# Performance work log

Hardware: AMD Instinct MI355X
Metric: run time of the kernel (lower is better)

## Reference

```python
import jax, jax.numpy as jnp
import numpy as np

EPS = 1e-5
COMMIT_W = 2.0
LATENT = 64


def _conv1d(x, w, b, stride, padding):
    # x: [B,C,T], w: [O,I,K] (torch Conv1d layout)
    y = jax.lax.conv_general_dilated(x, w, (stride,), [(padding, padding)],
                                     dimension_numbers=('NCH', 'OIH', 'NCH'))
    return y + b[None, :, None]


def _bn(x, g, b):
    # training-mode BatchNorm1d: batch statistics over (B, T) per channel
    mu = x.mean(axis=(0, 2), keepdims=True)
    var = x.var(axis=(0, 2), keepdims=True)
    return (x - mu) * jax.lax.rsqrt(var + EPS) * g[None, :, None] + b[None, :, None]


def setup_inputs():
    key = jax.random.key(0)
    ks = jax.random.split(key, 10)
    B, T, D, K = 8, 10240, LATENT, 8192
    f32 = jnp.float32
    def n(k, shape, scale):
        return jax.random.normal(k, shape, dtype=f32) * scale
    return {
        'x': jax.random.normal(ks[0], (B, 1, T), dtype=f32),
        'enc_w1': n(ks[1], (16, 1, 5), 0.3), 'enc_b1': jnp.zeros((16,), f32),
        'bn1_g': jnp.ones((16,), f32), 'bn1_b': jnp.zeros((16,), f32),
        'enc_w2': n(ks[2], (32, 16, 5), 0.1), 'enc_b2': jnp.zeros((32,), f32),
        'bn2_g': jnp.ones((32,), f32), 'bn2_b': jnp.zeros((32,), f32),
        'enc_w3': n(ks[3], (64, 32, 25), 0.05), 'enc_b3': jnp.zeros((64,), f32),
        'bn3_g': jnp.ones((64,), f32), 'bn3_b': jnp.zeros((64,), f32),
        'codebook': jax.random.normal(ks[4], (K, D), dtype=f32),
        'dec_wt': n(ks[5], (64, 64, 25), 0.05),  # torch ConvTranspose1d [in,out,k]
        'dbn1_g': jnp.ones((64,), f32), 'dbn1_b': jnp.zeros((64,), f32),
        'dec_w2': n(ks[6], (64, 64, 5), 0.08), 'dec_b2': jnp.zeros((64,), f32),
        'dbn2_g': jnp.ones((64,), f32), 'dbn2_b': jnp.zeros((64,), f32),
        'dec_w3': n(ks[7], (1, 64, 1), 0.1), 'dec_b3': jnp.zeros((1,), f32),
    }


def reference(x, enc_w1, enc_b1, bn1_g, bn1_b, enc_w2, enc_b2, bn2_g, bn2_b,
              enc_w3, enc_b3, bn3_g, bn3_b, codebook, dec_wt, dbn1_g, dbn1_b,
              dec_w2, dec_b2, dbn2_g, dbn2_b, dec_w3, dec_b3):
    # ---- encoder ----
    h = jax.nn.silu(_conv1d(x, enc_w1, enc_b1, 1, 2))
    h = _bn(h, bn1_g, bn1_b)
    h = jax.nn.silu(_conv1d(h, enc_w2, enc_b2, 1, 2))
    h = _bn(h, bn2_g, bn2_b)
    h = jnp.tanh(_conv1d(h, enc_w3, enc_b3, 5, 12))
    z = _bn(h, bn3_g, bn3_b)                       # [B, 64, L]
    B, _, L = z.shape
    # ---- VQ: euclidean nearest-neighbor against codebook ----
    zf = z.transpose(0, 2, 1).reshape(-1, LATENT)  # [N, D]
    d = ((zf * zf).sum(-1, keepdims=True)
         - 2.0 * zf @ codebook.T
         + (codebook * codebook).sum(-1)[None, :])  # [N, K]
    idx = jnp.argmin(d, axis=-1)                   # [N]
    q = codebook[idx]                              # [N, D]
    commit_loss = COMMIT_W * jnp.mean((jax.lax.stop_gradient(q) - zf) ** 2)
    q_st = zf + jax.lax.stop_gradient(q - zf)      # straight-through
    zq = q_st.reshape(B, L, LATENT).transpose(0, 2, 1)  # [B, 64, L]
    # ---- decoder ----
    # ConvTranspose1d(k=25, s=5, p=12) == dilated conv with flipped kernel
    wconv = jnp.flip(dec_wt, -1).transpose(1, 0, 2)     # [out, in, k]
    h = jax.lax.conv_general_dilated(zq, wconv, (1,), [(12, 12)], lhs_dilation=(5,),
                                     dimension_numbers=('NCH', 'OIH', 'NCH'))
    h = jax.nn.silu(h)
    h = _bn(h, dbn1_g, dbn1_b)
    h = jax.nn.silu(_conv1d(h, dec_w2, dec_b2, 1, 2))
    h = _bn(h, dbn2_g, dbn2_b)
    recon = _conv1d(h, dec_w3, dec_b3, 1, 0)       # [B, 1, ~T]
    T = x.shape[2]
    cur = recon.shape[2]
    if cur > T:
        recon = recon[:, :, :T]
    elif cur < T:
        recon = jnp.pad(recon, ((0, 0), (0, 0), (0, T - cur)))
    return recon, idx.reshape(B, L), commit_loss
```

## Files before the change

kernel.cpp:

```cpp
#include <hip/hip_runtime.h>
#include <hip/hip_bf16.h>

#define DEV __device__ __forceinline__

typedef __attribute__((ext_vector_type(8))) short s8v;
typedef __attribute__((ext_vector_type(16))) float f32x16;
typedef __attribute__((address_space(1))) const unsigned int u32g;
typedef __attribute__((address_space(3))) unsigned int u32l;

DEV void gl_lds(const void* g, void* l){
  __builtin_amdgcn_global_load_lds((u32g*)g, (u32l*)l, 16, 0, 0);
}

DEV float siluf(float x){ return x / (1.f + expf(-x)); }

DEV float wredsum(float v){
  #pragma unroll
  for(int m = 32; m; m >>= 1) v += __shfl_xor(v, m);
  return v;
}

DEV unsigned short bf16rne(float f){
  unsigned int u = __float_as_uint(f);
  u += 0x7FFFu + ((u >> 16) & 1u);
  return (unsigned short)(u >> 16);
}
DEV float bf16tof(unsigned short h){ return __uint_as_float(((unsigned int)h) << 16); }

DEV unsigned umed3(unsigned a, unsigned b, unsigned c){
  unsigned d;
  asm("v_med3_u32 %0, %1, %2, %3" : "=v"(d) : "v"(a), "v"(b), "v"(c));
  return d;
}

#define S1 0
#define Q1 16
#define S2 32
#define Q2 64
#define S3 96
#define Q3 160
#define S4 224
#define Q4 288
#define S5 352
#define Q5 416
#define SLOSS 480
#define NSTATF 512

#define EPSQ 6u
#define NCHUNK 8

__global__ void k_prep(const float* ew3, const float* dwt, float* w3t, float* dwtt,
                       unsigned short* wb7){
  const int n1 = 64*32*25, n2 = 64*64*25;
  for(int i = blockIdx.x*blockDim.x + threadIdx.x; i < n1+n2; i += gridDim.x*blockDim.x){
    if(i < n1){
      int c = i/(32*25), r = i - c*(32*25), ii = r/25, k = r - ii*25;
      w3t[(ii*25 + k)*64 + c] = ew3[i];
    } else {
      int j = i - n1;
      int ii = j/(64*25), r = j - ii*(64*25), o = r/25, k = r - o*25;
      float w = dwt[j];
      dwtt[(ii*25 + k)*64 + o] = w;
      wb7[((size_t)(k*64 + o))*64 + ii] = bf16rne(w);
    }
  }
}

__global__ void k_prep2(const float* __restrict__ cb, unsigned short* __restrict__ cbsw,
                        float* __restrict__ cnw, float* __restrict__ cnw2,
                        unsigned short* __restrict__ cbb, int* cnt){
  if(blockIdx.x == 0 && threadIdx.x == 0) *cnt = 0;
  int j = blockIdx.x*256 + threadIdx.x;
  if(j < 8192){
    float nrm = 0.f;
    unsigned swz = (j & 15) << 4;
    char* rowp = (char*)cbsw + (size_t)j*256;
    #pragma unroll
    for(int k = 0; k < 64; k++){
      float x = cb[(size_t)j*64 + k];
      unsigned short hi = bf16rne(x);
      float lo = x - bf16tof(hi);
      *(unsigned short*)(rowp + (((unsigned)(2*k)) ^ swz)) = hi;
      *(unsigned short*)(rowp + (((unsigned)(128 + 2*k)) ^ swz)) = bf16rne(lo);
      cbb[(size_t)j*64 + k] = hi;
      nrm = fmaf(x, x, nrm);
    }
    cnw[j] = nrm;
    cnw2[j] = (nrm + 1024.f) * 256.f;
  }
}

__global__ void k1(const float* __restrict__ x, const float* __restrict__ w1,
                   const float* __restrict__ b1, float* __restrict__ h1, float* stats){
  __shared__ float xs[260];
  __shared__ float ssum[16], ssq[16];
  int tid = threadIdx.x, b = blockIdx.y, t0 = blockIdx.x*256;
  if(tid < 16){ ssum[tid] = 0.f; ssq[tid] = 0.f; }
  for(int i = tid; i < 260; i += 256){
    int t = t0 + i - 2;
    xs[i] = (t >= 0 && t < 10240) ? x[b*10240 + t] : 0.f;
  }
  __syncthreads();
  int t = t0 + tid;
  #pragma unroll
  for(int c = 0; c < 16; c++){
    float a = b1[c];
    #pragma unroll
    for(int k = 0; k < 5; k++) a = fmaf(w1[c*5+k], xs[tid+k], a);
    a = siluf(a);
    h1[((b*16 + c)*10240) + t] = a;
    float s = wredsum(a), s2 = wredsum(a*a);
    if((tid & 63) == 0){ atomicAdd(&ssum[c], s); atomicAdd(&ssq[c], s2); }
  }
  __syncthreads();
  if(tid < 16){ atomicAdd(stats+S1+tid, ssum[tid]); atomicAdd(stats+Q1+tid, ssq[tid]); }
}

__global__ void k2(const float* __restrict__ h1, const float* __restrict__ w2,
                   const float* __restrict__ b2, const float* __restrict__ g1,
                   const float* __restrict__ bb1, float* __restrict__ h2out, float* stats){
  __shared__ float hs[16*264];
  __shared__ float wl[2560];
  __shared__ float A1[16], B1[16];
  __shared__ float ssum[32], ssq[32];
  int tid = threadIdx.x, b = blockIdx.y, t0 = blockIdx.x*256;
  for(int i = tid; i < 2560; i += 256) wl[i] = w2[i];
  if(tid < 16){
    float mu = stats[S1+tid]/81920.f;
    float var = stats[Q1+tid]/81920.f - mu*mu;
    float rs = rsqrtf(var + 1e-5f);
    A1[tid] = rs*g1[tid];
    B1[tid] = bb1[tid] - mu*rs*g1[tid];
  }
  if(tid < 32){ ssum[tid] = 0.f; ssq[tid] = 0.f; }
  __syncthreads();
  for(int i = tid; i < 16*260; i += 256){
    int ch = i/260, tt = i - ch*260;
    int t = t0 + tt - 2;
    hs[ch*264 + tt] = (t >= 0 && t < 10240) ? (h1[((b*16+ch)*10240)+t]*A1[ch] + B1[ch]) : 0.f;
  }
  __syncthreads();
  int t = t0 + tid;
  float acc[32];
  #pragma unroll
  for(int c = 0; c < 32; c++) acc[c] = b2[c];
  for(int i = 0; i < 16; i++){
    float z0 = hs[i*264+tid], z1 = hs[i*264+tid+1], z2 = hs[i*264+tid+2],
          z3 = hs[i*264+tid+3], z4 = hs[i*264+tid+4];
    #pragma unroll
    for(int c = 0; c < 32; c++){
      const float* wp = &wl[(c*16+i)*5];
      acc[c] = fmaf(wp[0],z0,fmaf(wp[1],z1,fmaf(wp[2],z2,fmaf(wp[3],z3,fmaf(wp[4],z4,acc[c])))));
    }
  }
  #pragma unroll
  for(int c = 0; c < 32; c++){
    float a = siluf(acc[c]);
    h2out[((b*32 + c)*10240) + t] = a;
    float s = wredsum(a), s2 = wredsum(a*a);
    if((tid & 63) == 0){ atomicAdd(&ssum[c], s); atomicAdd(&ssq[c], s2); }
  }
  __syncthreads();
  if(tid < 32){ atomicAdd(stats+S2+tid, ssum[tid]); atomicAdd(stats+Q2+tid, ssq[tid]); }
}

__global__ void k3(const float* __restrict__ h2, const float* __restrict__ w3t,
                   const float* __restrict__ eb3, const float* __restrict__ g2,
                   const float* __restrict__ bb2, float* __restrict__ zn, float* stats){
  __shared__ __align__(16) float X[5*32*24];
  __shared__ float A2[32], B2[32];
  __shared__ float ssum[64], ssq[64];
  int tid = threadIdx.x, b = blockIdx.y, l0 = blockIdx.x*16;
  if(tid < 32){
    float mu = stats[S2+tid]/81920.f;
    float var = stats[Q2+tid]/81920.f - mu*mu;
    float rs = rsqrtf(var + 1e-5f);
    A2[tid] = rs*g2[tid];
    B2[tid] = bb2[tid] - mu*rs*g2[tid];
  }
  if(tid < 64){ ssum[tid] = 0.f; ssq[tid] = 0.f; }
  __syncthreads();
  for(int i2 = tid; i2 < 5*32*20; i2 += 256){
    int kk = i2/640;
    int r  = i2 - kk*640;
    int ch = r/20, m = r - ch*20;
    int t = 5*(l0 + m) + kk - 12;
    float v = 0.f;
    if(t >= 0 && t < 10240) v = h2[((b*32+ch)*10240)+t]*A2[ch] + B2[ch];
    X[(kk*32+ch)*24 + m] = v;
  }
  __syncthreads();
  int c = tid & 63, lslot = tid >> 6;
  float acc[4];
  float bias = eb3[c];
  #pragma unroll
  for(int s = 0; s < 4; s++) acc[s] = bias;
  for(int i = 0; i < 32; i++){
    #pragma unroll
    for(int kk = 0; kk < 5; kk++){
      const float* xp = &X[(kk*32+i)*24 + lslot*4];
      float4 za = *(const float4*)(xp);
      float4 zb = *(const float4*)(xp + 4);
      float z[8] = {za.x,za.y,za.z,za.w,zb.x,zb.y,zb.z,zb.w};
      #pragma unroll
      for(int kap = 0; kap < 5; kap++){
        float w = w3t[(i*25 + kap*5 + kk)*64 + c];
        #pragma unroll
        for(int s = 0; s < 4; s++) acc[s] = fmaf(w, z[s+kap], acc[s]);
      }
    }
  }
  float ls = 0.f, lq = 0.f;
  #pragma unroll
  for(int s = 0; s < 4; s++){
    int l = l0 + lslot*4 + s;
    float a = tanhf(acc[s]);
    zn[((b*2048 + l)*64) + c] = a;
    ls += a; lq += a*a;
  }
  atomicAdd(&ssum[c], ls); atomicAdd(&ssq[c], lq);
  __syncthreads();
  if(tid < 64){ atomicAdd(stats+S3+tid, ssum[tid]); atomicAdd(stats+Q3+tid, ssq[tid]); }
}

__global__ void k3b(float* zn, const float* g3, const float* b3, const float* stats){
  __shared__ float A[64], B[64];
  int tid = threadIdx.x;
  if(tid < 64){
    float mu = stats[S3+tid]/16384.f;
    float var = stats[Q3+tid]/16384.f - mu*mu;
    float rs = rsqrtf(var + 1e-5f);
    A[tid] = rs*g3[tid];
    B[tid] = b3[tid] - mu*rs*g3[tid];
  }
  __syncthreads();
  for(int i = blockIdx.x*256 + tid; i < 16384*64; i += gridDim.x*256){
    int c = i & 63;
    zn[i] = zn[i]*A[c] + B[c];
  }
}

__global__ __launch_bounds__(256, 3) void k5m(const float* __restrict__ zn,
    const unsigned short* __restrict__ cbsw, const float* __restrict__ cnw2,
    unsigned int* __restrict__ pbk, unsigned int* __restrict__ psk){
  __shared__ __align__(16) unsigned char cbuf[2][16384];
  int tid = threadIdx.x;
  int chunk = blockIdx.x;
  int m0 = blockIdx.y * 128;
  int lane = tid & 63, wr = tid >> 6;
  int h = lane >> 5, cll = lane & 31;
  int row = m0 + wr*32 + cll;

  s8v ah[4], al[4];
  const float* zp = zn + (size_t)row*64;
  #pragma unroll
  for(int s = 0; s < 4; s++){
    float4 v0 = *(const float4*)(zp + s*16 + h*8);
    float4 v1 = *(const float4*)(zp + s*16 + h*8 + 4);
    float vv[8] = {v0.x,v0.y,v0.z,v0.w,v1.x,v1.y,v1.z,v1.w};
    #pragma unroll
    for(int i = 0; i < 8; i++){
      unsigned short hi = bf16rne(vv[i]);
      ah[s][i] = (short)hi;
      al[s][i] = (short)bf16rne(vv[i] - bf16tof(hi));
    }
  }

  unsigned int bk[16], sk[16];
  #pragma unroll
  for(int r = 0; r < 16; r++){ bk[r] = 0xFFFFFFFFu; sk[r] = 0xFFFFFFFFu; }
  f32x16 zv;
  #pragma unroll
  for(int i = 0; i < 16; i++) zv[i] = 0.f;

  int c0 = chunk * 1024;
  const char* csrc = (const char*)cbsw + (size_t)c0*256;
  #pragma unroll
  for(int c2 = 0; c2 < 4; c2++)
    gl_lds(csrc + c2*4096 + tid*16, &cbuf[0][0] + c2*4096 + tid*16);
  __syncthreads();

  unsigned swz = (unsigned)(cll & 15) << 4;
  for(int tile = 0; tile < 16; ++tile){
    int bsel = tile & 1;
    if(tile < 15){
      const char* ns = csrc + (size_t)(tile+1)*16384;
      #pragma unroll
      for(int c2 = 0; c2 < 4; c2++)
        gl_lds(ns + c2*4096 + tid*16, &cbuf[bsel^1][0] + c2*4096 + tid*16);
    }
    #pragma unroll
    for(int half = 0; half < 2; half++){
      const unsigned char* bp = &cbuf[bsel][0] + (half*32 + cll)*256;
      s8v bh[4], bl[4];
      #pragma unroll
      for(int s = 0; s < 4; s++){
        bh[s] = *(const s8v*)(bp + (((unsigned)(s*32 + h*16)) ^ swz));
        bl[s] = *(const s8v*)(bp + (((unsigned)(128 + s*32 + h*16)) ^ swz));
      }
      unsigned col = (unsigned)(c0 + tile*64 + half*32 + cll);
      float cnv2 = cnw2[col];
      f32x16 a1 = __builtin_amdgcn_mfma_f32_32x32x16_bf16(ah[0], bh[0], zv, 0, 0, 0);
      f32x16 a2 = __builtin_amdgcn_mfma_f32_32x32x16_bf16(al[0], bh[0], zv, 0, 0, 0);
      a2 = __builtin_amdgcn_mfma_f32_32x32x16_bf16(ah[0], bl[0], a2, 0, 0, 0);
      #pragma unroll
      for(int s = 1; s < 4; s++){
        a1 = __builtin_amdgcn_mfma_f32_32x32x16_bf16(ah[s], bh[s], a1, 0, 0, 0);
        a2 = __builtin_amdgcn_mfma_f32_32x32x16_bf16(al[s], bh[s], a2, 0, 0, 0);
        a2 = __builtin_amdgcn_mfma_f32_32x32x16_bf16(ah[s], bl[s], a2, 0, 0, 0);
      }
      #pragma unroll
      for(int r = 0; r < 16; r++){
        float q = fmaf(-512.f, a1[r], cnv2);
        q = fmaf(-512.f, a2[r], q);
        q = fminf(q, 524287.f);
        unsigned k = (((unsigned)q) << 13) | col;
        unsigned nb = bk[r] < k ? bk[r] : k;
        sk[r] = umed3(sk[r], bk[r], k);
        bk[r] = nb;
      }
    }
    __syncthreads();
  }

  #pragma unroll
  for(int m = 1; m <= 16; m <<= 1){
    #pragma unroll
    for(int r = 0; r < 16; r++){
      unsigned int ob = (unsigned int)__shfl_xor((int)bk[r], m);
      unsigned int os = (unsigned int)__shfl_xor((int)sk[r], m);
      unsigned int s2 = sk[r] < os ? sk[r] : os;
      sk[r] = umed3(s2, bk[r], ob);
      bk[r] = bk[r] < ob ? bk[r] : ob;
    }
  }
  if(cll == 0){
    size_t base = (size_t)chunk*16384 + m0 + wr*32 + 4*h;
    #pragma unroll
    for(int r = 0; r < 16; r++){
      int lr = (r&3) + 8*(r>>2);
      pbk[base + lr] = bk[r];
      psk[base + lr] = sk[r];
    }
  }
}

__global__ void k5r(const unsigned int* __restrict__ pbk,
                    const unsigned int* __restrict__ psk, int* __restrict__ idxw,
                    float* __restrict__ out_idx, int* __restrict__ list, int* cnt){
  int row = blockIdx.x*256 + threadIdx.x;
  unsigned int bk = pbk[row], sk = psk[row];
  #pragma unroll
  for(int c = 1; c < NCHUNK; c++){
    unsigned int ob = pbk[(size_t)c*16384 + row];
    unsigned int os = psk[(size_t)c*16384 + row];
    unsigned int s2 = sk < os ? sk : os;
    sk = umed3(s2, bk, ob);
    bk = bk < ob ? bk : ob;
  }
  int idx = (int)(bk & 0x1FFFu);
  idxw[row] = idx;
  out_idx[row] = (float)idx;
  if((sk >> 13) - (bk >> 13) <= EPSQ){
    int p = atomicAdd(cnt, 1);
    list[p] = row;
  }
}

__global__ __launch_bounds__(256) void k5x(const float* __restrict__ zn,
    const float* __restrict__ cb, const float* __restrict__ cnw,
    const int* __restrict__ list, const int* cnt,
    float* __restrict__ pxd, int* __restrict__ pxi){
  int tid = threadIdx.x;
  int chunk = blockIdx.x;
  int n = *cnt;
  int rgrp = tid >> 6, cs = tid & 63;
  int c0 = chunk * 1024;
  for(int bat = blockIdx.y; bat*4 < n; bat += 256){
    int e = bat*4 + rgrp;
    int ec = e < n ? e : n-1;
    int row = list[ec];
    float4 zr[16];
    const float4* zp = (const float4*)(zn + (size_t)row*64);
    #pragma unroll
    for(int q = 0; q < 16; q++) zr[q] = zp[q];
    float bd = 3.4e38f; int bi = 0;
    for(int step = 0; step < 16; step++){
      int j = c0 + step*64 + cs;
      const float4* cp = (const float4*)(cb + (size_t)j*64);
      float cnv = cnw[j];
      float da = 0.f, db = 0.f;
      #pragma unroll
      for(int q = 0; q < 16; q += 2){
        float4 ca = cp[q], cb4 = cp[q+1];
        da = fmaf(ca.x, zr[q].x, da);  da = fmaf(ca.y, zr[q].y, da);
        da = fmaf(ca.z, zr[q].z, da);  da = fmaf(ca.w, zr[q].w, da);
        db = fmaf(cb4.x, zr[q+1].x, db); db = fmaf(cb4.y, zr[q+1].y, db);
        db = fmaf(cb4.z, zr[q+1].z, db); db = fmaf(cb4.w, zr[q+1].w, db);
      }
      float d = fmaf(-2.f, da + db, cnv);
      if(d < bd){ bd = d; bi = j; }
    }
    #pragma unroll
    for(int m = 1; m <= 32; m <<= 1){
      float od = __shfl_xor(bd, m);
      int   oi = __shfl_xor(bi, m);
      if(od < bd || (od == bd && oi < bi)){ bd = od; bi = oi; }
    }
    if(cs == 0 && e < n){
      pxd[(size_t)chunk*16384 + e] = bd;
      pxi[(size_t)chunk*16384 + e] = bi;
    }
  }
}

__global__ void k5x2(const float* __restrict__ pxd, const int* __restrict__ pxi,
                     const int* __restrict__ list, const int* cnt,
                     int* __restrict__ idxw, float* __restrict__ out_idx){
  int e = blockIdx.x*256 + threadIdx.x;
  int n = *cnt;
  if(e >= n) return;
  float bd = pxd[e]; int bi = pxi[e];
  #pragma unroll
  for(int c = 1; c < NCHUNK; c++){
    float od = pxd[(size_t)c*16384 + e];
    int   oi = pxi[(size_t)c*16384 + e];
    if(od < bd || (od == bd && oi < bi)){ bd = od; bi = oi; }
  }
  int row = list[e];
  idxw[row] = bi;
  out_idx[row] = (float)bi;
}

__global__ void k_loss(const float* __restrict__ zn, const float* __restrict__ cb,
                       const int* __restrict__ idxw, float* stats){
  int row = blockIdx.x*256 + threadIdx.x;
  int code = idxw[row];
  const float* cp = cb + (size_t)code*64;
  const float* zp = zn + (size_t)row*64;
  float s = 0.f;
  #pragma unroll
  for(int k = 0; k < 64; k++){
    float dd = cp[k] - zp[k];
    s = fmaf(dd, dd, s);
  }
  float tot = wredsum(s);
  if((threadIdx.x & 63) == 0) atomicAdd(stats + SLOSS, tot);
}

__global__ __launch_bounds__(320) void k7m(const int* __restrict__ idxp,
    const unsigned short* __restrict__ cbb, const unsigned short* __restrict__ wb7,
    unsigned short* __restrict__ h4t, float* stats){
  __shared__ __align__(16) unsigned char lA[37*128];
  __shared__ float tb[5*64*33];
  __shared__ float ssum[64], ssq[64];
  int tid = threadIdx.x, b = blockIdx.y, u0 = blockIdx.x*32;
  if(tid < 64){ ssum[tid] = 0.f; ssq[tid] = 0.f; }
  {
    int m = tid >> 3, part = tid & 7;
    if(m < 37){
      int u = u0 - 2 + m;
      uint4 val = make_uint4(0,0,0,0);
      if(u >= 0 && u < 2048){
        int code = idxp[b*2048 + u];
        val = *(const uint4*)((const char*)cbb + (size_t)code*128 + part*16);
      }
      *(uint4*)(lA + m*128 + (((unsigned)(part*16)) ^ (((unsigned)m & 7) << 4))) = val;
    }
  }
  __syncthreads();
  int lane = tid & 63, h = lane >> 5, cl = lane & 31;
  int v = tid >> 6;
  const int km[5]  = {2,3,4,0,1};
  const int ovv[5] = {2,2,2,3,3};
  f32x16 acc0, acc1;
  #pragma unroll
  for(int i = 0; i < 16; i++){ acc0[i] = 0.f; acc1[i] = 0.f; }
  #pragma unroll
  for(int r = 0; r < 5; r++){
    int off = ovv[v] - r + 2;
    int m = cl + off;
    unsigned aswz = ((unsigned)m & 7) << 4;
    int k = km[v] + 5*r;
    const char* b0p = (const char*)wb7 + (size_t)(k*64 + cl)*128;
    const char* b1p = b0p + 32*128;
    #pragma unroll
    for(int s = 0; s < 4; s++){
      unsigned o = (unsigned)(s*32 + h*16);
      s8v a  = *(const s8v*)(lA + m*128 + (o ^ aswz));
      s8v b0 = *(const s8v*)(b0p + o);
      s8v b1 = *(const s8v*)(b1p + o);
      acc0 = __builtin_amdgcn_mfma_f32_32x32x16_bf16(a, b0, acc0, 0, 0, 0);
      acc1 = __builtin_amdgcn_mfma_f32_32x32x16_bf16(a, b1, acc1, 0, 0, 0);
    }
  }
  float ps0 = 0.f, pq0 = 0.f, ps1 = 0.f, pq1 = 0.f;
  #pragma unroll
  for(int r = 0; r < 16; r++){
    int ul = (r&3) + 8*(r>>2) + 4*h;
    int u = u0 + ul;
    float v0 = siluf(acc0[r]), v1 = siluf(acc1[r]);
    tb[(v*64 + cl)*33 + ul]      = v0;
    tb[(v*64 + 32 + cl)*33 + ul] = v1;
    if(v == 0 || u < 2047){ ps0 += v0; pq0 += v0*v0; ps1 += v1; pq1 += v1*v1; }
  }
  atomicAdd(&ssum[cl], ps0);      atomicAdd(&ssq[cl], pq0);
  atomicAdd(&ssum[32 + cl], ps1); atomicAdd(&ssq[32 + cl], pq1);
  __syncthreads();
  if(tid < 64){ atomicAdd(stats+S4+tid, ssum[tid]); atomicAdd(stats+Q4+tid, ssq[tid]); }
  #pragma unroll
  for(int j = 0; j < 16; j++){
    int flat = j*320 + tid;
    int tl = flat >> 5;
    int chp = flat & 31;
    int t = u0*5 + tl;
    if(t < 10236){
      int vv = tl % 5, ul = tl / 5;
      float f0 = tb[(vv*64 + 2*chp)*33 + ul];
      float f1 = tb[(vv*64 + 2*chp + 1)*33 + ul];
      unsigned int pk = (unsigned int)bf16rne(f0) | ((unsigned int)bf16rne(f1) << 16);
      size_t rowb = ((size_t)b*10248 + 2 + t)*128;
      *(unsigned int*)((char*)h4t + rowb + (((unsigned)(4*chp)) ^ (((unsigned)t & 7) << 4))) = pk;
    }
  }
}

__global__ void k8w(const float* __restrict__ w2d, const float* __restrict__ b2d,
                    const float* __restrict__ g4, const float* __restrict__ bb4,
                    const float* __restrict__ stats, unsigned short* __restrict__ wbt,
                    float* __restrict__ beta, unsigned int* __restrict__ h4tz){
  __shared__ float A4[64], B4[64];
  int tid = threadIdx.x;
  for(int i = tid; i < 3072; i += 256){
    int b = i / 384, r = i - b*384;
    int row12 = r >> 5, word = r & 31;
    int row = row12 < 2 ? row12 : 10236 + row12;
    h4tz[((size_t)b*10248 + row)*32 + word] = 0u;
  }
  if(tid < 64){
    float mu = stats[S4+tid]/81888.f;
    float var = stats[Q4+tid]/81888.f - mu*mu;
    float rs = rsqrtf(var + 1e-5f);
    A4[tid] = rs*g4[tid];
    B4[tid] = bb4[tid] - mu*rs*g4[tid];
  }
  __syncthreads();
  for(int e = tid; e < 64*64*5; e += 256){
    int c = e/320, r = e - c*320, i = r/5, k = r - i*5;
    unsigned short hw = bf16rne(w2d[e] * A4[i]);
    int row = k*64 + c;
    *(unsigned short*)((char*)wbt + (size_t)row*128 + (((unsigned)(2*i)) ^ (((unsigned)c & 7) << 4))) = hw;
  }
  if(tid < 64){
    float s = b2d[tid];
    for(int i = 0; i < 64; i++){
      float wsum = 0.f;
      #pragma unroll
      for(int k = 0; k < 5; k++) wsum += w2d[(tid*64 + i)*5 + k];
      s += wsum * B4[i];
    }
    beta[tid] = s;
  }
}

__global__ __launch_bounds__(256) void k8(const unsigned short* __restrict__ h4t,
    const unsigned short* __restrict__ wbt, const float* __restrict__ beta,
    unsigned short* __restrict__ h5b, float* stats){
  __shared__ __align__(16) unsigned char lA[68*128];
  __shared__ float ssum[64], ssq[64];
  int tid = threadIdx.x, b = blockIdx.y, t0 = blockIdx.x*64;
  if(tid < 64){ ssum[tid] = 0.f; ssq[tid] = 0.f; }
  const char* srcA = (const char*)h4t + ((size_t)b*10248 + t0)*128;
  #pragma unroll
  for(int c2 = 0; c2 < 2; c2++)
    gl_lds(srcA + c2*4096 + tid*16, lA + c2*4096 + tid*16);
  if(tid < 32) gl_lds(srcA + 8192 + tid*16, lA + 8192 + tid*16);
  __syncthreads();

  int lane = tid & 63, h = lane >> 5, cl = lane & 31;
  int widx = tid >> 6;
  int wt0 = (widx >> 1) * 32;
  int wch = (widx & 1) * 32;
  f32x16 acc;
  #pragma unroll
  for(int i = 0; i < 16; i++) acc[i] = 0.f;
  unsigned bswz = (unsigned)(cl & 7) << 4;
  #pragma unroll
  for(int k = 0; k < 5; k++){
    int l = wt0 + cl + k;
    unsigned aswz = (unsigned)((l + 6) & 7) << 4;
    const char* bp = (const char*)wbt + (size_t)(k*64 + wch + cl)*128;
    #pragma unroll
    for(int s = 0; s < 4; s++){
      unsigned o = (unsigned)(s*32 + h*16);
      s8v a  = *(const s8v*)(lA + l*128 + (o ^ aswz));
      s8v bb = *(const s8v*)(bp + (o ^ bswz));
      acc = __builtin_amdgcn_mfma_f32_32x32x16_bf16(a, bb, acc, 0, 0, 0);
    }
  }
  float bet = beta[wch + cl];
  float ps = 0.f, pq = 0.f;
  #pragma unroll
  for(int r = 0; r < 16; r++){
    int t = t0 + wt0 + (r&3) + 8*(r>>2) + 4*h;
    float v0 = siluf(acc[r] + bet);
    if(t < 10236){
      h5b[((size_t)b*10240 + t)*64 + wch + cl] = bf16rne(v0);
      ps += v0; pq += v0*v0;
    }
  }
  atomicAdd(&ssum[wch + cl], ps); atomicAdd(&ssq[wch + cl], pq);
  __syncthreads();
  if(tid < 64){ atomicAdd(stats+S5+tid, ssum[tid]); atomicAdd(stats+Q5+tid, ssq[tid]); }
}

__global__ void k9(const unsigned short* __restrict__ h5b, const float* __restrict__ w3,
                   const float* __restrict__ b3, const float* __restrict__ g5,
                   const float* __restrict__ bb5, const float* stats,
                   float* __restrict__ out){
  __shared__ float WA[64], WB[64];
  int tid = threadIdx.x;
  if(blockIdx.x == 0 && blockIdx.y == 0 && tid == 0)
    out[98304] = 2.f * stats[SLOSS] / 1048576.f;
  if(tid < 64){
    float mu = stats[S5+tid]/81888.f;
    float var = stats[Q5+tid]/81888.f - mu*mu;
    float rs = rsqrtf(var + 1e-5f);
    float A = rs*g5[tid], B = bb5[tid] - mu*rs*g5[tid];
    float w = w3[tid];
    WA[tid] = w*A; WB[tid] = w*B;
  }
  __syncthreads();
  int b = blockIdx.y;
  int t = blockIdx.x*256 + tid;
  float acc = b3[0];
  if(t < 10236){
    const unsigned short* hp = h5b + ((size_t)b*10240 + t)*64;
    #pragma unroll
    for(int q = 0; q < 8; q++){
      uint4 u = *(const uint4*)(hp + q*8);
      unsigned int ua[4] = {u.x, u.y, u.z, u.w};
      #pragma unroll
      for(int w = 0; w < 4; w++){
        int c = q*8 + w*2;
        acc += WA[c]*bf16tof((unsigned short)(ua[w] & 0xFFFFu)) + WB[c];
        acc += WA[c+1]*bf16tof((unsigned short)(ua[w] >> 16)) + WB[c+1];
      }
    }
  } else acc = 0.f;
  out[b*10240 + t] = acc;
}

extern "C" void kernel_launch(void* const* d_in, const int* in_sizes, int n_in,
                              void* d_out, int out_size, void* d_ws, size_t ws_size,
                              hipStream_t stream){
  const float* x   = (const float*)d_in[0];
  const float* ew1 = (const float*)d_in[1];
  const float* eb1 = (const float*)d_in[2];
  const float* g1  = (const float*)d_in[3];
  const float* bb1 = (const float*)d_in[4];
  const float* ew2 = (const float*)d_in[5];
  const float* eb2 = (const float*)d_in[6];
  const float* g2  = (const float*)d_in[7];
  const float* bb2 = (const float*)d_in[8];
  const float* ew3 = (const float*)d_in[9];
  const float* eb3 = (const float*)d_in[10];
  const float* g3  = (const float*)d_in[11];
  const float* bb3 = (const float*)d_in[12];
  const float* cb  = (const float*)d_in[13];
  const float* dwt = (const float*)d_in[14];
  const float* g4  = (const float*)d_in[15];
  const float* bb4 = (const float*)d_in[16];
  const float* w2d = (const float*)d_in[17];
  const float* b2d = (const float*)d_in[18];
  const float* g5  = (const float*)d_in[19];
  const float* bb5 = (const float*)d_in[20];
  const float* w3d = (const float*)d_in[21];
  const float* b3d = (const float*)d_in[22];

  char* ws = (char*)d_ws;
  float* h1   = (float*)(ws + 0);
  unsigned short* cbsw = (unsigned short*)(ws + 0);
  float* cnw  = (float*)(ws + 2097152);
  float* cnw2 = (float*)(ws + 2129920);
  float* h2   = (float*)(ws + 5242880);
  float* zn   = (float*)(ws + 15728640);
  unsigned short* h4t = (unsigned short*)(ws + 0);
  unsigned short* h5b = (unsigned short*)(ws + 20971520);
  int*   list = (int*)  (ws + 20971520);
  int*   cnt  = (int*)  (ws + 21037056);
  unsigned int* pbk = (unsigned int*)(ws + 21037312);
  unsigned int* psk = (unsigned int*)(ws + 21561600);
  float* pxd  = (float*)(ws + 22085888);
  int*   pxi  = (int*)  (ws + 22610176);
  unsigned short* wbt = (unsigned short*)(ws + 31457280);
  float* beta = (float*)(ws + 31498240);
  unsigned short* wb7 = (unsigned short*)(ws + 32000000);
  unsigned short* cbb = (unsigned short*)(ws + 32300032);
  float* w3t  = (float*)(ws + 41934848);
  float* dwtt = (float*)(ws + 42139648);
  int*   idxw = (int*)  (ws + 42549248);
  float* stats= (float*)(ws + 42614784);
  if(ws_size < 42616832) return;

  float* out = (float*)d_out;

  hipMemsetAsync(stats, 0, NSTATF*4, stream);
  k_prep<<<600, 256, 0, stream>>>(ew3, dwt, w3t, dwtt, wb7);
  k1<<<dim3(40,8), 256, 0, stream>>>(x, ew1, eb1, h1, stats);
  k2<<<dim3(40,8), 256, 0, stream>>>(h1, ew2, eb2, g1, bb1, h2, stats);
  k_prep2<<<32, 256, 0, stream>>>(cb, cbsw, cnw, cnw2, cbb, cnt);
  k3<<<dim3(128,8), 256, 0, stream>>>(h2, w3t, eb3, g2, bb2, zn, stats);
  k3b<<<1024, 256, 0, stream>>>(zn, g3, bb3, stats);
  k5m<<<dim3(NCHUNK,128), 256, 0, stream>>>(zn, cbsw, cnw2, pbk, psk);
  k5r<<<64, 256, 0, stream>>>(pbk, psk, idxw, out + 81920, list, cnt);
  k5x<<<dim3(NCHUNK,256), 256, 0, stream>>>(zn, cb, cnw, list, cnt, pxd, pxi);
  k5x2<<<64, 256, 0, stream>>>(pxd, pxi, list, cnt, idxw, out + 81920);
  k_loss<<<64, 256, 0, stream>>>(zn, cb, idxw, stats);
  k7m<<<dim3(64,8), 320, 0, stream>>>(idxw, cbb, wb7, h4t, stats);
  k8w<<<1, 256, 0, stream>>>(w2d, b2d, g4, bb4, stats, wbt, beta, (unsigned int*)h4t);
  k8<<<dim3(160,8), 256, 0, stream>>>(h4t, wbt, beta, h5b, stats);
  k9<<<dim3(40,8), 256, 0, stream>>>(h5b, w3d, b3d, g5, bb5, stats, out);
}
```

Before: 389.0 us.

## Remap encoder conv kernels to channel-per-thread with register-blocked time outputs

k1 and k2 change their thread mapping. Each thread now owns one output channel and computes a strip of consecutive time samples (8 in k1, 16 in k2), held in registers and written with float4 stores. Tiles shrink to 128 samples and the grid doubles to 80 blocks per batch. k2 reads its weights directly from global memory as float4 instead of staging them in LDS, and BN statistics are reduced with fewer shuffles and atomics. Separately, k5m's launch-bounds occupancy hint rises from 3 to 4 waves, which may cause register spills in that kernel.

Result: faster. 360.5 us (-7.3%).

```diff
diff --git a/kernel.cpp b/kernel.cpp
--- a/kernel.cpp
+++ b/kernel.cpp
@@ -92,74 +92,106 @@
 
 __global__ void k1(const float* __restrict__ x, const float* __restrict__ w1,
                    const float* __restrict__ b1, float* __restrict__ h1, float* stats){
-  __shared__ float xs[260];
+  __shared__ float xs[136];
   __shared__ float ssum[16], ssq[16];
-  int tid = threadIdx.x, b = blockIdx.y, t0 = blockIdx.x*256;
+  int tid = threadIdx.x, b = blockIdx.y, t0 = blockIdx.x*128;
   if(tid < 16){ ssum[tid] = 0.f; ssq[tid] = 0.f; }
-  for(int i = tid; i < 260; i += 256){
+  for(int i = tid; i < 132; i += 256){
     int t = t0 + i - 2;
     xs[i] = (t >= 0 && t < 10240) ? x[b*10240 + t] : 0.f;
   }
   __syncthreads();
-  int t = t0 + tid;
-  #pragma unroll
-  for(int c = 0; c < 16; c++){
-    float a = b1[c];
-    #pragma unroll
-    for(int k = 0; k < 5; k++) a = fmaf(w1[c*5+k], xs[tid+k], a);
+  int c = tid & 15, sgrp = tid >> 4;
+  float w[5];
+  #pragma unroll
+  for(int k = 0; k < 5; k++) w[k] = w1[c*5 + k];
+  float bias = b1[c];
+  float outv[8];
+  float ps = 0.f, pq = 0.f;
+  #pragma unroll
+  for(int s = 0; s < 8; s++){
+    float a = bias;
+    #pragma unroll
+    for(int k = 0; k < 5; k++) a = fmaf(w[k], xs[sgrp*8 + s + k], a);
     a = siluf(a);
-    h1[((b*16 + c)*10240) + t] = a;
-    float s = wredsum(a), s2 = wredsum(a*a);
-    if((tid & 63) == 0){ atomicAdd(&ssum[c], s); atomicAdd(&ssq[c], s2); }
-  }
+    outv[s] = a;
+    ps += a; pq += a*a;
+  }
+  float* op = h1 + ((size_t)(b*16 + c))*10240 + t0 + sgrp*8;
+  #pragma unroll
+  for(int q = 0; q < 2; q++)
+    *(float4*)(op + q*4) = make_float4(outv[q*4], outv[q*4+1], outv[q*4+2], outv[q*4+3]);
+  ps += __shfl_xor(ps, 16); pq += __shfl_xor(pq, 16);
+  ps += __shfl_xor(ps, 32); pq += __shfl_xor(pq, 32);
+  if((tid & 48) == 0){ atomicAdd(&ssum[c], ps); atomicAdd(&ssq[c], pq); }
   __syncthreads();
   if(tid < 16){ atomicAdd(stats+S1+tid, ssum[tid]); atomicAdd(stats+Q1+tid, ssq[tid]); }
 }
 
-__global__ void k2(const float* __restrict__ h1, const float* __restrict__ w2,
-                   const float* __restrict__ b2, const float* __restrict__ g1,
-                   const float* __restrict__ bb1, float* __restrict__ h2out, float* stats){
-  __shared__ float hs[16*264];
-  __shared__ float wl[2560];
-  __shared__ float A1[16], B1[16];
+__global__ __launch_bounds__(256) void k2(const float* __restrict__ h1,
+                   const float* __restrict__ w2, const float* __restrict__ b2,
+                   const float* __restrict__ g1, const float* __restrict__ bb1,
+                   float* __restrict__ h2out, float* stats){
+  __shared__ float hs[16][136];
+  __shared__ float A1s[16], B1s[16];
   __shared__ float ssum[32], ssq[32];
-  int tid = threadIdx.x, b = blockIdx.y, t0 = blockIdx.x*256;
-  for(int i = tid; i < 2560; i += 256) wl[i] = w2[i];
+  int tid = threadIdx.x, b = blockIdx.y, t0 = blockIdx.x*128;
   if(tid < 16){
     float mu = stats[S1+tid]/81920.f;
     float var = stats[Q1+tid]/81920.f - mu*mu;
     float rs = rsqrtf(var + 1e-5f);
-    A1[tid] = rs*g1[tid];
-    B1[tid] = bb1[tid] - mu*rs*g1[tid];
+    A1s[tid] = rs*g1[tid];
+    B1s[tid] = bb1[tid] - mu*rs*g1[tid];
   }
   if(tid < 32){ ssum[tid] = 0.f; ssq[tid] = 0.f; }
   __syncthreads();
-  for(int i = tid; i < 16*260; i += 256){
-    int ch = i/260, tt = i - ch*260;
-    int t = t0 + tt - 2;
-    hs[ch*264 + tt] = (t >= 0 && t < 10240) ? (h1[((b*16+ch)*10240)+t]*A1[ch] + B1[ch]) : 0.f;
-  }
-  __syncthreads();
-  int t = t0 + tid;
-  float acc[32];
-  #pragma unroll
-  for(int c = 0; c < 32; c++) acc[c] = b2[c];
-  for(int i = 0; i < 16; i++){
-    float z0 = hs[i*264+tid], z1 = hs[i*264+tid+1], z2 = hs[i*264+tid+2],
-          z3 = hs[i*264+tid+3], z4 = hs[i*264+tid+4];
-    #pragma unroll
-    for(int c = 0; c < 32; c++){
-      const float* wp = &wl[(c*16+i)*5];
-      acc[c] = fmaf(wp[0],z0,fmaf(wp[1],z1,fmaf(wp[2],z2,fmaf(wp[3],z3,fmaf(wp[4],z4,acc[c])))));
-    }
-  }
-  #pragma unroll
-  for(int c = 0; c < 32; c++){
-    float a = siluf(acc[c]);
-    h2out[((b*32 + c)*10240) + t] = a;
-    float s = wredsum(a), s2 = wredsum(a*a);
-    if((tid & 63) == 0){ atomicAdd(&ssum[c], s); atomicAdd(&ssq[c], s2); }
-  }
+  {
+    int ch = tid >> 4, j0 = tid & 15;
+    float A = A1s[ch], B = B1s[ch];
+    const float* hp = h1 + ((size_t)(b*16 + ch))*10240;
+    for(int j = j0; j < 132; j += 16){
+      int t = t0 + j - 2;
+      hs[ch][j] = (t >= 0 && t < 10240) ? hp[t]*A + B : 0.f;
+    }
+  }
+  __syncthreads();
+  int c = tid & 31, tgrp = tid >> 5;
+  int tb = tgrp*16;
+  float acc[16];
+  float bias = b2[c];
+  #pragma unroll
+  for(int s = 0; s < 16; s++) acc[s] = bias;
+  for(int ic = 0; ic < 4; ic++){
+    float wf[20];
+    const float* wp = w2 + c*80 + ic*20;
+    #pragma unroll
+    for(int q = 0; q < 5; q++) *(float4*)(wf + q*4) = *(const float4*)(wp + q*4);
+    #pragma unroll
+    for(int di = 0; di < 4; di++){
+      int i = ic*4 + di;
+      float z[20];
+      #pragma unroll
+      for(int q = 0; q < 5; q++) *(float4*)(z + q*4) = *(const float4*)(&hs[i][tb] + q*4);
+      float w0 = wf[di*5], w1 = wf[di*5+1], w2v = wf[di*5+2], w3 = wf[di*5+3], w4 = wf[di*5+4];
+      #pragma unroll
+      for(int s = 0; s < 16; s++)
+        acc[s] = fmaf(w0, z[s], fmaf(w1, z[s+1], fmaf(w2v, z[s+2],
+                 fmaf(w3, z[s+3], fmaf(w4, z[s+4], acc[s])))));
+    }
+  }
+  float ps = 0.f, pq = 0.f;
+  #pragma unroll
+  for(int s = 0; s < 16; s++){
+    float a = siluf(acc[s]);
+    acc[s] = a;
+    ps += a; pq += a*a;
+  }
+  float* op = h2out + ((size_t)(b*32 + c))*10240 + t0 + tb;
+  #pragma unroll
+  for(int q = 0; q < 4; q++)
+    *(float4*)(op + q*4) = make_float4(acc[q*4], acc[q*4+1], acc[q*4+2], acc[q*4+3]);
+  ps += __shfl_xor(ps, 32); pq += __shfl_xor(pq, 32);
+  if((tid & 32) == 0){ atomicAdd(&ssum[c], ps); atomicAdd(&ssq[c], pq); }
   __syncthreads();
   if(tid < 32){ atomicAdd(stats+S2+tid, ssum[tid]); atomicAdd(stats+Q2+tid, ssq[tid]); }
 }
@@ -240,7 +272,7 @@
   }
 }
 
-__global__ __launch_bounds__(256, 3) void k5m(const float* __restrict__ zn,
+__global__ __launch_bounds__(256, 4) void k5m(const float* __restrict__ zn,
     const unsigned short* __restrict__ cbsw, const float* __restrict__ cnw2,
     unsigned int* __restrict__ pbk, unsigned int* __restrict__ psk){
   __shared__ __align__(16) unsigned char cbuf[2][16384];
@@ -707,8 +739,8 @@
 
   hipMemsetAsync(stats, 0, NSTATF*4, stream);
   k_prep<<<600, 256, 0, stream>>>(ew3, dwt, w3t, dwtt, wb7);
-  k1<<<dim3(40,8), 256, 0, stream>>>(x, ew1, eb1, h1, stats);
-  k2<<<dim3(40,8), 256, 0, stream>>>(h1, ew2, eb2, g1, bb1, h2, stats);
+  k1<<<dim3(80,8), 256, 0, stream>>>(x, ew1, eb1, h1, stats);
+  k2<<<dim3(80,8), 256, 0, stream>>>(h1, ew2, eb2, g1, bb1, h2, stats);
   k_prep2<<<32, 256, 0, stream>>>(cb, cbsw, cnw, cnw2, cbb, cnt);
   k3<<<dim3(128,8), 256, 0, stream>>>(h2, w3t, eb3, g2, bb2, zn, stats);
   k3b<<<1024, 256, 0, stream>>>(zn, g3, bb3, stats);
```
